# Kernel tuning notes

Measured on AMD Instinct MI355X. Metric: run time of the kernel, lower is better.

## Reference

```python
import jax, jax.numpy as jnp
import numpy as np

B, S, HID = 1, 2048, 4096
NH, NKV, HD = 32, 8, 128
WINDOW = 1024
ROPE_THETA = 1e6
NEG = -1e9


def rotate_half(x):
    x1, x2 = jnp.split(x, 2, axis=-1)
    return jnp.concatenate((-x2, x1), axis=-1)


def setup_inputs() -> dict:
    key = jax.random.key(0)
    ks = jax.random.split(key, 10)
    hidden_states = jax.random.normal(ks[0], (B, S, HID), jnp.float32)
    # rotary tables [max_pos, head_dim]
    inv_freq = 1.0 / (ROPE_THETA ** (jnp.arange(0, HD, 2, dtype=jnp.float32) / HD))
    t = jnp.arange(S, dtype=jnp.float32)
    freqs = jnp.outer(t, inv_freq)                       # [S, HD/2]
    emb = jnp.concatenate((freqs, freqs), axis=-1)       # [S, HD]
    cos, sin = jnp.cos(emb), jnp.sin(emb)
    position_ids = jnp.arange(S, dtype=jnp.int64)[None, :].astype(jnp.int32)
    # sliding-window causal additive mask [B,1,S,S]
    i = jnp.arange(S)[:, None]
    j = jnp.arange(S)[None, :]
    allowed = (j <= i) & (j > i - WINDOW)
    attention_mask = jnp.where(allowed, 0.0, NEG).astype(jnp.float32)[None, None]
    sc = 0.02
    Wq = jax.random.normal(ks[1], (HID, NH * HD), jnp.float32) * sc
    bq = jax.random.normal(ks[2], (NH * HD,), jnp.float32) * sc
    Wk = jax.random.normal(ks[3], (HID, NKV * HD), jnp.float32) * sc
    bk = jax.random.normal(ks[4], (NKV * HD,), jnp.float32) * sc
    Wv = jax.random.normal(ks[5], (HID, NKV * HD), jnp.float32) * sc
    bv = jax.random.normal(ks[6], (NKV * HD,), jnp.float32) * sc
    Wo = jax.random.normal(ks[7], (NH * HD, HID), jnp.float32) * sc
    bo = jax.random.normal(ks[8], (HID,), jnp.float32) * sc
    return dict(hidden_states=hidden_states, attention_mask=attention_mask,
                position_ids=position_ids, cos=cos, sin=sin,
                Wq=Wq, bq=bq, Wk=Wk, bk=bk, Wv=Wv, bv=bv, Wo=Wo, bo=bo)


def reference(hidden_states, attention_mask, position_ids, cos, sin,
              Wq, bq, Wk, bk, Wv, bv, Wo, bo):
    bsz, q_len, _ = hidden_states.shape
    q = (hidden_states @ Wq + bq).reshape(bsz, q_len, NH, HD).transpose(0, 2, 1, 3)
    k = (hidden_states @ Wk + bk).reshape(bsz, q_len, NKV, HD).transpose(0, 2, 1, 3)
    v = (hidden_states @ Wv + bv).reshape(bsz, q_len, NKV, HD).transpose(0, 2, 1, 3)
    # RoPE: cos/sin gathered by position_ids -> [B,1,S,HD]
    c = cos[position_ids][:, None]
    s = sin[position_ids][:, None]
    q = q * c + rotate_half(q) * s
    k = k * c + rotate_half(k) * s
    # GQA repeat_kv: [B,NKV,S,HD] -> [B,NH,S,HD]
    n_rep = NH // NKV
    k = jnp.repeat(k, n_rep, axis=1)
    v = jnp.repeat(v, n_rep, axis=1)
    scores = jnp.einsum('bhqd,bhkd->bhqk', q, k) / np.sqrt(HD).astype(np.float32)
    scores = scores + attention_mask[:, :, :, :k.shape[2]]
    probs = jax.nn.softmax(scores.astype(jnp.float32), axis=-1).astype(q.dtype)
    attn = jnp.einsum('bhqk,bhkd->bhqd', probs, v)
    attn = attn.transpose(0, 2, 1, 3).reshape(bsz, q_len, NH * HD)
    return attn @ Wo + bo
```

## Files before the change

### kernel.cpp

```cpp
#include <hip/hip_runtime.h>
#include <stdint.h>

typedef unsigned short u16;
typedef __attribute__((ext_vector_type(4))) float f32x4;
typedef __attribute__((ext_vector_type(16))) float f32x16;
typedef __attribute__((ext_vector_type(8))) __bf16 bf16x8;
typedef __attribute__((ext_vector_type(4))) u16 u16x4;
typedef __attribute__((ext_vector_type(8))) u16 u16x8;
typedef __attribute__((ext_vector_type(4))) unsigned int u32x4;

#define S_LEN 2048
#define HIDDEN 4096
#define NHEAD 32
#define NKVH 8
#define HD 128
#define WIN 1024

__device__ __forceinline__ float bf2f(u16 u) {
  union { unsigned int i; float f; } x; x.i = ((unsigned int)u) << 16; return x.f;
}
__device__ __forceinline__ u16 f2bf(float f) {
  union { float f; unsigned int i; } x; x.f = f;
  unsigned int r = x.i + 0x7FFFu + ((x.i >> 16) & 1u);
  return (u16)(r >> 16);
}

__device__ __forceinline__ void gload16(const void* g, void* l) {
  __builtin_amdgcn_global_load_lds((const __attribute__((address_space(1))) void*)g,
                                   (__attribute__((address_space(3))) void*)l, 16, 0, 0);
}

__device__ __forceinline__ unsigned int cvtpk_bf16(float a, float b) {
  unsigned int w;
  asm("v_cvt_pk_bf16_f32 %0, %1, %2" : "=v"(w) : "v"(a), "v"(b));
  return w;
}

__device__ __forceinline__ void transp_f32(const float* __restrict__ in, int istride,
                                           u16* __restrict__ out, int ostride,
                                           int bx, int by, char* smem) {
  float (*tile)[68] = (float (*)[68])smem;
  int r0 = bx * 64, c0 = by * 64;
  int t = threadIdx.x;
  int tr = t >> 4;
  int tc = (t & 15) * 4;
#pragma unroll
  for (int i = 0; i < 4; ++i) {
    int r = i * 16 + tr;
    *(f32x4*)&tile[r][tc] = *(const f32x4*)(in + (size_t)(r0 + r) * istride + c0 + tc);
  }
  __syncthreads();
#pragma unroll
  for (int i = 0; i < 4; ++i) {
    int rr = i * 16 + tr;
    u16x4 o;
#pragma unroll
    for (int j = 0; j < 4; ++j) o[j] = f2bf(tile[tc + j][rr]);
    *(u16x4*)(out + (size_t)(c0 + rr) * ostride + r0 + tc) = o;
  }
}

__global__ __launch_bounds__(256) void prep_k(const float* __restrict__ X,
                                              const float* __restrict__ Wq, const float* __restrict__ Wk,
                                              const float* __restrict__ Wv,
                                              const float* __restrict__ bq, const float* __restrict__ bk,
                                              const float* __restrict__ bv,
                                              u16* __restrict__ Xb, u16* __restrict__ WT,
                                              float* __restrict__ bqkv) {
  __shared__ __align__(16) char smem[17408];
  int bid = blockIdx.x;
  if (bid < 4096) {
    size_t i = ((size_t)bid * 256 + threadIdx.x) * 8;
    f32x4 a = *(const f32x4*)(X + i);
    f32x4 b = *(const f32x4*)(X + i + 4);
    u16x8 o;
    o[0] = f2bf(a[0]); o[1] = f2bf(a[1]); o[2] = f2bf(a[2]); o[3] = f2bf(a[3]);
    o[4] = f2bf(b[0]); o[5] = f2bf(b[1]); o[6] = f2bf(b[2]); o[7] = f2bf(b[3]);
    *(u16x8*)(Xb + i) = o;
  } else if (bid < 8192) {
    int tt = bid - 4096;
    transp_f32(Wq, 4096, WT, 4096, tt & 63, tt >> 6, smem);
  } else if (bid < 9216) {
    int tt = bid - 8192;
    transp_f32(Wk, 1024, WT + (size_t)4096 * 4096, 4096, tt & 63, tt >> 6, smem);
  } else if (bid < 10240) {
    int tt = bid - 9216;
    transp_f32(Wv, 1024, WT + (size_t)5120 * 4096, 4096, tt & 63, tt >> 6, smem);
  } else {
    int i = (bid - 10240) * 256 + threadIdx.x;
    float v = (i < 4096) ? bq[i] : (i < 5120 ? bk[i - 4096] : bv[i - 5120]);
    bqkv[i] = v;
  }
}

__global__ __launch_bounds__(256) void mid_k(const u16* __restrict__ qkv, const int* __restrict__ pos,
                                             const float* __restrict__ cosT, const float* __restrict__ sinT,
                                             u16* __restrict__ Q, u16* __restrict__ Kf, u16* __restrict__ Vf,
                                             const float* __restrict__ Wo, u16* __restrict__ WT) {
  __shared__ __align__(16) char smem[17408];
  int bid = blockIdx.x;
  if (bid < 20480) {
    int p = bid * 256 + threadIdx.x;
    int s = p / 2560;
    int rem = p - s * 2560;
    int hs = rem >> 6;
    int d = rem & 63;
    int ps = pos[s];
    const float* cb = cosT + (size_t)ps * 128;
    const float* sb = sinT + (size_t)ps * 128;
    float c0 = cb[d], c1 = cb[d + 64], s0 = sb[d], s1 = sb[d + 64];
    if (hs < NHEAD) {
      const u16* src = qkv + (size_t)s * 6144 + hs * 128;
      float x0 = bf2f(src[d]), x1 = bf2f(src[d + 64]);
      const float qs = 0.08838834764831845f;
      u16* dst = Q + ((size_t)hs * S_LEN + s) * HD;
      dst[d] = f2bf((x0 * c0 - x1 * s0) * qs);
      dst[d + 64] = f2bf((x1 * c1 + x0 * s1) * qs);
    } else {
      int kh = hs - NHEAD;
      const u16* src = qkv + (size_t)s * 6144 + 4096 + kh * 128;
      float x0 = bf2f(src[d]), x1 = bf2f(src[d + 64]);
      int t = s >> 5, cr = s & 31;
      int ks = d >> 4, hi2 = (d >> 3) & 1, j = d & 7;
      size_t base = ((size_t)(kh * 64 + t) * 8 + ks) * 512 + (size_t)(cr + 32 * hi2) * 8 + j;
      Kf[base] = f2bf(x0 * c0 - x1 * s0);
      Kf[base + 4 * 512] = f2bf(x1 * c1 + x0 * s1);
    }
  } else if (bid < 20992) {
    u16 (*tile)[136] = (u16 (*)[136])smem;
    int b2 = bid - 20480;
    int kh = b2 >> 6, t = b2 & 63;
    int tid = threadIdx.x;
#pragma unroll
    for (int i = 0; i < 2; ++i) {
      int c = tid + i * 256;
      int r = c >> 4, seg = c & 15;
      *(u16x8*)&tile[r][seg * 8] =
          *(const u16x8*)(qkv + (size_t)(t * 32 + r) * 6144 + 5120 + kh * 128 + seg * 8);
    }
    __syncthreads();
#pragma unroll
    for (int i = 0; i < 2; ++i) {
      int pp = tid + i * 256;
      int dt = pp >> 7, sl = (pp >> 6) & 1, l = pp & 63;
      int c2 = l & 31, h2 = l >> 5;
      u16x8 o;
#pragma unroll
      for (int j = 0; j < 8; ++j) o[j] = tile[sl * 16 + h2 * 8 + j][dt * 32 + c2];
      *(u16x8*)(Vf + ((size_t)(kh * 512 + t * 8 + dt * 2 + sl)) * 512 + (size_t)l * 8) = o;
    }
  } else {
    int tt = bid - 20992;
    transp_f32(Wo, 4096, WT, 4096, tt & 63, tt >> 6, smem);
  }
}

template <int BM, int BN, int MINW, typename TOUT>
__global__ __launch_bounds__(256, MINW) void gemm4_k(const u16* __restrict__ A, const u16* __restrict__ Bt,
                                                     const float* __restrict__ bias, TOUT* __restrict__ C,
                                                     int M, int N, int K) {
  constexpr int WM = BM / 2, WN = BN / 2;
  constexpr int MRA = WM / 16, MRB = WN / 16;
  constexpr int NA = BM / 64, NB = BN / 64;
  constexpr int NL = NA + NB;
  __shared__ __align__(16) u16 SA[3 * BM * 32];
  __shared__ __align__(16) u16 SB[3 * BN * 32];

  int tid = threadIdx.x;
  int w = tid >> 6, l = tid & 63;
  int cl = l & 15, g = l >> 4;
  int wr = w >> 1, wc = w & 1;

  int cpx = gridDim.x >> 3;
  int wg = (blockIdx.x & 7) * cpx + (blockIdx.x >> 3);
  int nbm = M / BM;
  int bm = wg % nbm, bn = wg / nbm;

  const u16* Ag = A + (size_t)(bm * BM) * K;
  const u16* Bg = Bt + (size_t)(bn * BN) * K;
  int srow = w * 16 + (l >> 2);
  int csrc = ((l & 3) ^ ((l >> 3) & 3)) * 8;
  int rdc = (g ^ ((cl >> 1) & 3)) << 3;

  f32x4 acc[MRA][MRB] = {};
  int NT = K >> 5;

  auto stage = [&](int slot, int tt, int h) {
    if (h < NA) {
      gload16(Ag + (size_t)(h * 64 + srow) * K + tt * 32 + csrc,
              (void*)(SA + slot * (BM * 32) + (h * 64 + w * 16) * 32));
    } else {
      int hb = h - NA;
      gload16(Bg + (size_t)(hb * 64 + srow) * K + tt * 32 + csrc,
              (void*)(SB + slot * (BN * 32) + (hb * 64 + w * 16) * 32));
    }
  };

#pragma unroll
  for (int h = 0; h < NL; ++h) stage(0, 0, h);
#pragma unroll
  for (int h = 0; h < NL; ++h) stage(1, 1, h);

  for (int t = 0; t < NT; ++t) {
    if constexpr (NL == 5) asm volatile("s_waitcnt vmcnt(5)" ::: "memory");
    else if constexpr (NL == 4) asm volatile("s_waitcnt vmcnt(4)" ::: "memory");
    else asm volatile("s_waitcnt vmcnt(3)" ::: "memory");
    __builtin_amdgcn_s_barrier();
    asm volatile("" ::: "memory");

    int slot = t % 3, ss = (t + 2) % 3;
    int ts = t + 2; if (ts >= NT) ts -= NT;
#pragma unroll
    for (int h = 0; h < NL; ++h) stage(ss, ts, h);

    const u16* sa = SA + slot * (BM * 32);
    const u16* sb = SB + slot * (BN * 32);
    bf16x8 af[MRA], bf[MRB];
#pragma unroll
    for (int mi = 0; mi < MRA; ++mi)
      af[mi] = *(const bf16x8*)(sa + (wr * WM + mi * 16 + cl) * 32 + rdc);
#pragma unroll
    for (int ni = 0; ni < MRB; ++ni)
      bf[ni] = *(const bf16x8*)(sb + (wc * WN + ni * 16 + cl) * 32 + rdc);
    __builtin_amdgcn_s_setprio(1);
#pragma unroll
    for (int mi = 0; mi < MRA; ++mi)
#pragma unroll
      for (int ni = 0; ni < MRB; ++ni)
        acc[mi][ni] = __builtin_amdgcn_mfma_f32_16x16x32_bf16(af[mi], bf[ni], acc[mi][ni], 0, 0, 0);
    __builtin_amdgcn_s_setprio(0);
  }

  asm volatile("s_waitcnt vmcnt(0)" ::: "memory");

#pragma unroll
  for (int mi = 0; mi < MRA; ++mi) {
    int row0 = bm * BM + wr * WM + mi * 16 + g * 4;
#pragma unroll
    for (int ni = 0; ni < MRB; ++ni) {
      int col = bn * BN + wc * WN + ni * 16 + cl;
      float bb = bias[col];
      f32x4 a = acc[mi][ni];
#pragma unroll
      for (int r = 0; r < 4; ++r) {
        float v = a[r] + bb;
        if constexpr (sizeof(TOUT) == 2) C[(size_t)(row0 + r) * N + col] = f2bf(v);
        else C[(size_t)(row0 + r) * N + col] = v;
      }
    }
  }
}

__global__ __launch_bounds__(256, 2) void attn_k(const u16* __restrict__ Q, const u16* __restrict__ Kf,
                                                 const u16* __restrict__ Vf, u16* __restrict__ O) {
  int l = threadIdx.x & 63, w = threadIdx.x >> 6;
  int col = l & 31, hi = l >> 5;
  int bid = blockIdx.x;
  int kh = bid & 7;
  int head = (bid >> 3) & 3;
  int qbp = bid >> 5;
  int qb = (qbp & 1) ? (15 - (qbp >> 1)) : (qbp >> 1);
  int h = kh * 4 + head;
  int q0 = qb * 128 + w * 32;

  bf16x8 qf[8];
  const u16* qbase = Q + ((size_t)h * S_LEN + q0 + col) * HD + hi * 8;
#pragma unroll
  for (int ks = 0; ks < 8; ++ks) qf[ks] = *(const bf16x8*)(qbase + ks * 16);

  f32x16 ot[4];
#pragma unroll
  for (int dt = 0; dt < 4; ++dt)
#pragma unroll
    for (int r = 0; r < 16; ++r) ot[dt][r] = 0.f;
  float m_r = -3.0e38f, l_r = 0.f;

  const u16* kf0 = Kf + (size_t)kh * 64 * 4096 + (size_t)l * 8;
  const u16* vf0 = Vf + (size_t)kh * 512 * 512 + (size_t)l * 8;

  int jstart = q0 >= WIN ? q0 - WIN : 0;
  bf16x8 kfr[8];
  {
    const u16* kb = kf0 + (size_t)(jstart >> 5) * 4096;
#pragma unroll
    for (int ks = 0; ks < 8; ++ks) kfr[ks] = *(const bf16x8*)(kb + ks * 512);
  }

  for (int j0 = jstart; j0 <= q0; j0 += 32) {
    int t = j0 >> 5;
    f32x16 sA = {}, sB = {};
#pragma unroll
    for (int ks = 0; ks < 4; ++ks)
      sA = __builtin_amdgcn_mfma_f32_32x32x16_bf16(kfr[ks], qf[ks], sA, 0, 0, 0);
#pragma unroll
    for (int ks = 4; ks < 8; ++ks)
      sB = __builtin_amdgcn_mfma_f32_32x32x16_bf16(kfr[ks], qf[ks], sB, 0, 0, 0);
    int tn = (j0 + 32 <= q0) ? (t + 1) : t;
    const u16* kbn = kf0 + (size_t)tn * 4096;
    bf16x8 kfn[8];
#pragma unroll
    for (int ks = 0; ks < 8; ++ks) kfn[ks] = *(const bf16x8*)(kbn + ks * 512);
    const u16* vb = vf0 + (size_t)t * 4096;
    bf16x8 vfr[8];
#pragma unroll
    for (int c = 0; c < 8; ++c) vfr[c] = *(const bf16x8*)(vb + c * 512);

    f32x16 s = sA + sB;

    if (j0 + 31 > q0 || j0 < q0 - 992) {
      int q = q0 + col;
#pragma unroll
      for (int r = 0; r < 16; ++r) {
        int kv = j0 + (r & 3) + 8 * (r >> 2) + 4 * hi;
        if (kv > q || kv <= q - WIN) s[r] = -3.0e38f;
      }
    }
    float vm = fmaxf(fmaxf(fmaxf(s[0], s[1]), fmaxf(s[2], s[3])),
                     fmaxf(fmaxf(s[4], s[5]), fmaxf(s[6], s[7])));
    vm = fmaxf(vm, fmaxf(fmaxf(fmaxf(s[8], s[9]), fmaxf(s[10], s[11])),
                         fmaxf(fmaxf(s[12], s[13]), fmaxf(s[14], s[15]))));
    vm = fmaxf(vm, __shfl_xor(vm, 32));
    float mnew = fmaxf(m_r, vm);
    float sc = __expf(m_r - mnew);
    m_r = mnew;
    float rs = 0.f;
#pragma unroll
    for (int r = 0; r < 16; ++r) {
      float pv = __expf(s[r] - mnew);
      s[r] = pv;
      rs += pv;
    }
    rs += __shfl_xor(rs, 32);
    l_r = l_r * sc + rs;
#pragma unroll
    for (int dt = 0; dt < 4; ++dt)
#pragma unroll
      for (int r = 0; r < 16; ++r) ot[dt][r] *= sc;

    bf16x8 pb[2];
#pragma unroll
    for (int sl = 0; sl < 2; ++sl) {
      int b = sl * 8;
      unsigned int a0 = cvtpk_bf16(s[b + 0], s[b + 1]);
      unsigned int c0 = cvtpk_bf16(s[b + 4], s[b + 5]);
      asm("v_permlane32_swap_b32 %0, %1" : "+v"(a0), "+v"(c0));
      unsigned int a1 = cvtpk_bf16(s[b + 2], s[b + 3]);
      unsigned int c1 = cvtpk_bf16(s[b + 6], s[b + 7]);
      asm("v_permlane32_swap_b32 %0, %1" : "+v"(a1), "+v"(c1));
      u32x4 pv = {a0, a1, c0, c1};
      pb[sl] = __builtin_bit_cast(bf16x8, pv);
    }
#pragma unroll
    for (int dt = 0; dt < 4; ++dt) {
      ot[dt] = __builtin_amdgcn_mfma_f32_32x32x16_bf16(vfr[dt * 2 + 0], pb[0], ot[dt], 0, 0, 0);
      ot[dt] = __builtin_amdgcn_mfma_f32_32x32x16_bf16(vfr[dt * 2 + 1], pb[1], ot[dt], 0, 0, 0);
    }
#pragma unroll
    for (int ks = 0; ks < 8; ++ks) kfr[ks] = kfn[ks];
  }

  float inv = 1.0f / l_r;
#pragma unroll
  for (int dt = 0; dt < 4; ++dt) {
#pragma unroll
    for (int g2 = 0; g2 < 4; ++g2) {
      u16x4 o;
#pragma unroll
      for (int i = 0; i < 4; ++i) o[i] = f2bf(ot[dt][g2 * 4 + i] * inv);
      *(u16x4*)(O + (size_t)(q0 + col) * HIDDEN + h * HD + dt * 32 + g2 * 8 + hi * 4) = o;
    }
  }
}

extern "C" void kernel_launch(void* const* d_in, const int* in_sizes, int n_in,
                              void* d_out, int out_size, void* d_ws, size_t ws_size,
                              hipStream_t stream) {
  const float* X = (const float*)d_in[0];
  const int* pos = (const int*)d_in[2];
  const float* cosT = (const float*)d_in[3];
  const float* sinT = (const float*)d_in[4];
  const float* Wq = (const float*)d_in[5];
  const float* bq = (const float*)d_in[6];
  const float* Wk = (const float*)d_in[7];
  const float* bk = (const float*)d_in[8];
  const float* Wv = (const float*)d_in[9];
  const float* bv = (const float*)d_in[10];
  const float* Wo = (const float*)d_in[11];
  const float* bo = (const float*)d_in[12];
  float* out = (float*)d_out;

  const size_t MB = 1ull << 20;
  char* ws = (char*)d_ws;
  u16* WT = (u16*)ws;
  u16* Xb = (u16*)(ws + 48 * MB);
  u16* Qs = Xb;
  u16* QKVr = (u16*)(ws + 64 * MB);
  u16* attnO = QKVr;
  u16* Kfr = (u16*)(ws + 88 * MB);
  u16* Vfr = (u16*)(ws + 92 * MB);
  float* bqkv = (float*)(ws + 96 * MB);

  prep_k<<<10264, 256, 0, stream>>>(X, Wq, Wk, Wv, bq, bk, bv, Xb, WT, bqkv);

  gemm4_k<128, 128, 3, u16><<<768, 256, 0, stream>>>(Xb, WT, bqkv, QKVr, 2048, 6144, 4096);

  mid_k<<<25088, 256, 0, stream>>>(QKVr, pos, cosT, sinT, Qs, Kfr, Vfr, Wo, WT);

  attn_k<<<512, 256, 0, stream>>>(Qs, Kfr, Vfr, attnO);

  gemm4_k<64, 128, 4, float><<<1024, 256, 0, stream>>>(attnO, WT, bo, out, 2048, 4096, 4096);
}
```

Measured before the change: 345.3 us.

## Drop K/V register prefetch in attention, raise occupancy, retile output GEMM

The attention kernel no longer double-buffers K fragments and no longer preloads V tiles into registers. K and V are now loaded just before each MFMA, and the split sA/sB accumulators are merged into one. This frees registers so launch bounds can ask for 3 waves per SIMD instead of 2, trading explicit latency hiding for more occupancy. Separately, the output projection GEMM moves to 128x128 tiles with 3 stages and half as many blocks.

```diff
diff --git a/kernel.cpp b/kernel.cpp
--- a/kernel.cpp
+++ b/kernel.cpp
@@ -251,7 +251,7 @@
   }
 }
 
-__global__ __launch_bounds__(256, 2) void attn_k(const u16* __restrict__ Q, const u16* __restrict__ Kf,
+__global__ __launch_bounds__(256, 3) void attn_k(const u16* __restrict__ Q, const u16* __restrict__ Kf,
                                                  const u16* __restrict__ Vf, u16* __restrict__ O) {
   int l = threadIdx.x & 63, w = threadIdx.x >> 6;
   int col = l & 31, hi = l >> 5;
@@ -279,33 +279,15 @@
   const u16* vf0 = Vf + (size_t)kh * 512 * 512 + (size_t)l * 8;
 
   int jstart = q0 >= WIN ? q0 - WIN : 0;
-  bf16x8 kfr[8];
-  {
-    const u16* kb = kf0 + (size_t)(jstart >> 5) * 4096;
-#pragma unroll
-    for (int ks = 0; ks < 8; ++ks) kfr[ks] = *(const bf16x8*)(kb + ks * 512);
-  }
-
   for (int j0 = jstart; j0 <= q0; j0 += 32) {
     int t = j0 >> 5;
-    f32x16 sA = {}, sB = {};
-#pragma unroll
-    for (int ks = 0; ks < 4; ++ks)
-      sA = __builtin_amdgcn_mfma_f32_32x32x16_bf16(kfr[ks], qf[ks], sA, 0, 0, 0);
-#pragma unroll
-    for (int ks = 4; ks < 8; ++ks)
-      sB = __builtin_amdgcn_mfma_f32_32x32x16_bf16(kfr[ks], qf[ks], sB, 0, 0, 0);
-    int tn = (j0 + 32 <= q0) ? (t + 1) : t;
-    const u16* kbn = kf0 + (size_t)tn * 4096;
-    bf16x8 kfn[8];
-#pragma unroll
-    for (int ks = 0; ks < 8; ++ks) kfn[ks] = *(const bf16x8*)(kbn + ks * 512);
-    const u16* vb = vf0 + (size_t)t * 4096;
-    bf16x8 vfr[8];
-#pragma unroll
-    for (int c = 0; c < 8; ++c) vfr[c] = *(const bf16x8*)(vb + c * 512);
-
-    f32x16 s = sA + sB;
+    const u16* kb = kf0 + (size_t)t * 4096;
+    f32x16 s = {};
+#pragma unroll
+    for (int ks = 0; ks < 8; ++ks) {
+      bf16x8 kfr = *(const bf16x8*)(kb + ks * 512);
+      s = __builtin_amdgcn_mfma_f32_32x32x16_bf16(kfr, qf[ks], s, 0, 0, 0);
+    }
 
     if (j0 + 31 > q0 || j0 < q0 - 992) {
       int q = q0 + col;
@@ -350,13 +332,14 @@
       u32x4 pv = {a0, a1, c0, c1};
       pb[sl] = __builtin_bit_cast(bf16x8, pv);
     }
+    const u16* vb = vf0 + (size_t)t * 4096;
 #pragma unroll
     for (int dt = 0; dt < 4; ++dt) {
-      ot[dt] = __builtin_amdgcn_mfma_f32_32x32x16_bf16(vfr[dt * 2 + 0], pb[0], ot[dt], 0, 0, 0);
-      ot[dt] = __builtin_amdgcn_mfma_f32_32x32x16_bf16(vfr[dt * 2 + 1], pb[1], ot[dt], 0, 0, 0);
-    }
-#pragma unroll
-    for (int ks = 0; ks < 8; ++ks) kfr[ks] = kfn[ks];
+      bf16x8 v0 = *(const bf16x8*)(vb + (dt * 2 + 0) * 512);
+      bf16x8 v1 = *(const bf16x8*)(vb + (dt * 2 + 1) * 512);
+      ot[dt] = __builtin_amdgcn_mfma_f32_32x32x16_bf16(v0, pb[0], ot[dt], 0, 0, 0);
+      ot[dt] = __builtin_amdgcn_mfma_f32_32x32x16_bf16(v1, pb[1], ot[dt], 0, 0, 0);
+    }
   }
 
   float inv = 1.0f / l_r;
@@ -408,5 +391,5 @@
 
   attn_k<<<512, 256, 0, stream>>>(Qs, Kfr, Vfr, attnO);
 
-  gemm4_k<64, 128, 4, float><<<1024, 256, 0, stream>>>(attnO, WT, bo, out, 2048, 4096, 4096);
-}
+  gemm4_k<128, 128, 3, float><<<512, 256, 0, stream>>>(attnO, WT, bo, out, 2048, 4096, 4096);
+}
```

Result: slower. 359.9 us (+4.2%).
